# Kernel tuning notes

Hardware: AMD Instinct MI355X
Metric: run time of the kernel (lower is better)

## Reference

```python
import jax, jax.numpy as jnp
import numpy as np

N_ATOM = 30000
N_PAIR = 1_000_000
N_TRI = 4_000_000
N_SF = 16
RC = 6.0

LAMBD = jnp.array([-1.0, 1.0] * 8, dtype=jnp.float32)
ZETA = jnp.array([1.0, 1.0, 2.0, 2.0, 4.0, 4.0, 8.0, 8.0] * 2, dtype=jnp.float32)
ETA = jnp.array([0.01, 0.014, 0.02, 0.028, 0.04, 0.056, 0.08, 0.11,
                 0.16, 0.22, 0.32, 0.45, 0.63, 0.72, 0.9, 1.0], dtype=jnp.float32)


def cutoff_f1(r):
    # PiNN 'f1' cutoff: 0.5*(cos(pi*r/rc)+1)
    return 0.5 * (jnp.cos(jnp.float32(np.pi) * r / RC) + 1.0)


def gaussian_basis(r, fc):
    # GaussianBasis with center=0, gamma=eta: fc * exp(-eta * r^2), shape [n, n_sf]
    return fc[:, None] * jnp.exp(-ETA[None, :] * (r[:, None] ** 2))


def setup_inputs() -> dict:
    key = jax.random.key(0)
    k1, k2, k3, k4, k5 = jax.random.split(key, 5)
    ind_2 = jax.random.randint(k1, (N_PAIR, 2), 0, N_ATOM, dtype=jnp.int32)
    ind_3 = jax.random.randint(k2, (N_TRI, 2), 0, N_PAIR, dtype=jnp.int32)
    dist = jax.random.uniform(k3, (N_PAIR,), jnp.float32, 0.5, RC)
    dirs = jax.random.normal(k4, (N_PAIR, 3), jnp.float32)
    dirs = dirs / jnp.linalg.norm(dirs, axis=1, keepdims=True)
    diff = dirs * dist[:, None]  # bond vectors consistent with dist
    elems = jax.random.randint(k5, (N_ATOM,), 0, 4, dtype=jnp.int32)
    fc = cutoff_f1(dist)
    return {"ind_2": ind_2, "ind_3": ind_3, "dist": dist, "diff": diff,
            "elems": elems, "fc": fc}


def reference(ind_2, ind_3, dist, diff, elems, fc):
    # i=j=k='ALL': species filter is identity; a_rind = arange(n_atom)
    ind_ij = ind_3[:, 0]
    ind_ik = ind_3[:, 1]
    i_rind = ind_2[ind_ij, 0]  # central atom index per triplet

    diff_ij = diff[ind_ij]  # [T,3]
    diff_ik = diff[ind_ik]
    diff_jk = diff_ik - diff_ij
    dist_jk = jnp.linalg.norm(diff_jk, axis=1)
    mask = dist_jk < RC  # TF filters triplets; we mask (jit-friendly)

    fc_jk = cutoff_f1(dist_jk)
    dist_ij = dist[ind_ij]
    dist_ik = dist[ind_ik]
    fc_ij = fc[ind_ij]
    fc_ik = fc[ind_ik]

    cos_ijk = jnp.einsum('id,id->i', diff_ij, diff_ik) / dist_ij / dist_ik
    base = jnp.maximum(1.0 + LAMBD[None, :] * cos_ijk[:, None], 0.0)
    sf = (2.0 ** (1.0 - ZETA[None, :]) * base ** ZETA[None, :]
          * gaussian_basis(dist_ij, fc_ij)
          * gaussian_basis(dist_ik, fc_ik)
          * gaussian_basis(dist_jk, fc_jk))
    sf = jnp.where(mask[:, None], sf, 0.0)

    # scatter_nd add into per-atom fingerprints
    fp = jnp.zeros((N_ATOM, N_SF), dtype=sf.dtype).at[i_rind].add(sf)

    # jacobian indices: central-atom rel index per participating pair
    vals = jnp.where(mask, i_rind, -1)
    seg = jnp.concatenate([ind_ij, ind_ik])
    pair_i = jax.ops.segment_max(jnp.concatenate([vals, vals]), seg,
                                 num_segments=N_PAIR)
    pair_i = jnp.maximum(pair_i, -1)  # empty segments -> -1 sentinel
    jacob_ind = jnp.stack([jnp.arange(N_PAIR, dtype=jnp.int32), pair_i], axis=1)
    return fp, jacob_ind
```

## Files before the change

kernel.cpp:

```cpp
#include <hip/hip_runtime.h>

#define N_ATOM 30000
#define N_PAIR 1000000
#define N_TRI  4000000
#define N_SF   16
#define FP_ELEMS (N_ATOM * N_SF)

#define ASH  5
#define APB  32
#define NCB  938
#define NSUB 8
#define NSEG (NCB * NSUB)
#define OVF_CNT_IDX NSEG
#define OVF_CAP 131072
#define TILE 4096
#define PER_TH 16
#define NTILES ((N_TRI + TILE - 1) / TILE)
#define NWAVE 4

#define OFF_CCNT  0ULL
#define OFF_IKMAX 65536ULL
#define OFF_AOFP  4065536ULL
#define OFF_FLAG  6065536ULL
#define OFF_OVF   7065536ULL
#define OFF_PACK  8114112ULL
#define OFF_CB    24114112ULL

__device__ __forceinline__ bool tri_math_pack(
    float4 A, float4 B, float A8[8], float& R2)
{
    float ax = A.x, ay = A.y, az = A.z, fcij = A.w;
    float bx = B.x, by = B.y, bz = B.z, fcik = B.w;
    float d2ij = fmaf(ax, ax, fmaf(ay, ay, az * az));
    float d2ik = fmaf(bx, bx, fmaf(by, by, bz * bz));
    float jx = bx - ax, jy = by - ay, jz = bz - az;
    float d2jk = fmaf(jx, jx, fmaf(jy, jy, jz * jz));
    if (!(d2jk < 36.0f)) return false;
    float dij = sqrtf(d2ij);
    float dik = sqrtf(d2ik);
    float djk = sqrtf(d2jk);
    const float PI_OVER_RC = 0.5235987755982988f;
    float fcjk = 0.5f * (__cosf(PI_OVER_RC * djk) + 1.0f);
    float dot = fmaf(ax, bx, fmaf(ay, by, az * bz));
    float cosv = dot / (dij * dik);
    R2 = d2ij + d2ik + d2jk;
    float FCt = fcij * fcik * fcjk;
    float bm = fmaxf(1.0f - cosv, 0.0f);
    float bp = fmaxf(1.0f + cosv, 0.0f);
    float bm2 = bm * bm, bp2 = bp * bp;
    float bm4 = bm2 * bm2, bp4 = bp2 * bp2;
    float bm8 = bm4 * bm4, bp8 = bp4 * bp4;
    A8[0] = FCt * bm;              A8[1] = FCt * bp;
    A8[2] = 0.5f * FCt * bm2;      A8[3] = 0.5f * FCt * bp2;
    A8[4] = 0.125f * FCt * bm4;    A8[5] = 0.125f * FCt * bp4;
    A8[6] = 0.0078125f * FCt * bm8; A8[7] = 0.0078125f * FCt * bp8;
    return true;
}

#define SF_ACCUM(lrow, A8, R2, ATOMIC) do {                                   \
    float e0  = __expf(-0.01f  * (R2));                                       \
    float e1  = __expf(-0.014f * (R2));                                       \
    float e7  = __expf(-0.11f  * (R2));                                       \
    float e11 = __expf(-0.45f  * (R2));                                       \
    float e2 = e0*e0,  e3 = e1*e1;                                            \
    float e4 = e2*e2,  e5 = e3*e3;                                            \
    float e6 = e4*e4,  e9 = e7*e7;                                            \
    float e8 = e6*e6,  e14 = e11*e11;                                         \
    float e10 = e8*e8;                                                        \
    float e12 = e11*e8*e2;                                                    \
    float e13 = e10*e10*e6;                                                   \
    float e15 = e14*e6*e2;                                                    \
    ATOMIC(&(lrow)[0],  (A8)[0]*e0);  ATOMIC(&(lrow)[1],  (A8)[1]*e1);        \
    ATOMIC(&(lrow)[2],  (A8)[2]*e2);  ATOMIC(&(lrow)[3],  (A8)[3]*e3);        \
    ATOMIC(&(lrow)[4],  (A8)[4]*e4);  ATOMIC(&(lrow)[5],  (A8)[5]*e5);        \
    ATOMIC(&(lrow)[6],  (A8)[6]*e6);  ATOMIC(&(lrow)[7],  (A8)[7]*e7);        \
    ATOMIC(&(lrow)[8],  (A8)[0]*e8);  ATOMIC(&(lrow)[9],  (A8)[1]*e9);        \
    ATOMIC(&(lrow)[10], (A8)[2]*e10); ATOMIC(&(lrow)[11], (A8)[3]*e11);       \
    ATOMIC(&(lrow)[12], (A8)[4]*e12); ATOMIC(&(lrow)[13], (A8)[5]*e13);       \
    ATOMIC(&(lrow)[14], (A8)[6]*e14); ATOMIC(&(lrow)[15], (A8)[7]*e15);       \
} while (0)

#define ATOM_LDS(p, v)  atomicAdd((p), (v))
#define ATOM_GLB(p, v)  unsafeAtomicAdd((p), (v))


__global__ __launch_bounds__(256) void prep2(
    const int2* __restrict__ ind2, const float* __restrict__ diff,
    const float* __restrict__ fc,
    int* __restrict__ ccnt, int* __restrict__ ikmax,
    unsigned short* __restrict__ aofp, unsigned char* __restrict__ flag,
    float4* __restrict__ pack, float* __restrict__ out)
{
    int p = blockIdx.x * blockDim.x + threadIdx.x;
    if (p <= NSEG) ccnt[p] = 0;
    if (p < FP_ELEMS) out[p] = 0.0f;
    if (p >= N_PAIR) return;
    ikmax[p] = -1;
    flag[p] = 0;
    aofp[p] = (unsigned short)ind2[p].x;
    float4 r;
    r.x = diff[3 * p + 0];
    r.y = diff[3 * p + 1];
    r.z = diff[3 * p + 2];
    r.w = fc[p];
    pack[p] = r;
}

__global__ __launch_bounds__(256) void bin3(
    const int2* __restrict__ ind3, const unsigned short* __restrict__ aofp,
    int* __restrict__ ccnt, int2* __restrict__ cbucket,
    int2* __restrict__ ovf, int cap)
{
    __shared__ int lcnt[NCB];
    __shared__ int lbase[NCB];
    const int thr = threadIdx.x;
    const int sub = blockIdx.x & (NSUB - 1);
    const long long t0 = (long long)blockIdx.x * TILE;

    for (int i = thr; i < NCB; i += 256) lcnt[i] = 0;
    __syncthreads();

    int myatom[PER_TH];
    int myslot[PER_TH];
#pragma unroll
    for (int j = 0; j < PER_TH; ++j) {
        long long t = t0 + j * 256 + thr;
        int a = 0, s = -1;
        if (t < N_TRI) {
            int ij = ind3[t].x;
            a = aofp[ij];
            s = atomicAdd(&lcnt[a >> ASH], 1);
        }
        myatom[j] = a;
        myslot[j] = s;
    }
    __syncthreads();
    for (int c = thr; c < NCB; c += 256) {
        int n = lcnt[c];
        lbase[c] = n ? atomicAdd(&ccnt[c * NSUB + sub], n) : 0;
    }
    __syncthreads();
#pragma unroll
    for (int j = 0; j < PER_TH; ++j) {
        long long t = t0 + j * 256 + thr;
        if (t >= N_TRI) continue;
        int a = myatom[j];
        int c = a >> ASH;
        int slot = lbase[c] + myslot[j];
        int2 pr = ind3[t];
        if (slot < cap) {
            int2 e;
            e.x = pr.x | ((a & (APB - 1)) << 20);
            e.y = pr.y;
            cbucket[(size_t)(c * NSUB + sub) * cap + slot] = e;
        } else {
            int o = atomicAdd(&ccnt[OVF_CNT_IDX], 1);
            if (o < OVF_CAP) ovf[o] = pr;
        }
    }
}

__global__ __launch_bounds__(256) void reduce4(
    const int* __restrict__ ccnt, const int2* __restrict__ cbucket, int cap,
    const float4* __restrict__ pack,
    int* __restrict__ ikmax, unsigned char* __restrict__ flag,
    float* __restrict__ out)
{
    __shared__ float lacc[NWAVE][APB * 17];
    const int seg = blockIdx.x;
    const int b = seg >> 3;
    const int thr = threadIdx.x;
    const int wid = thr >> 6;
    for (int i = thr; i < NWAVE * APB * 17; i += 256)
        ((float*)lacc)[i] = 0.0f;
    __syncthreads();

    int n = ccnt[seg];
    n = min(n, cap);
    const int2* segp = cbucket + (size_t)seg * cap;
    for (int i = thr; i < n; i += 256) {
        int2 e = segp[i];
        int a5 = (e.x >> 20) & (APB - 1);
        int ij = e.x & 0xFFFFF;
        int ik = e.y;
        float4 A = pack[ij];
        float4 B = pack[ik];
        float A8[8], R2;
        if (!tri_math_pack(A, B, A8, R2)) continue;
        flag[ij] = 1;
        atomicMax(&ikmax[ik], (b << ASH) + a5);
        float* lrow = &lacc[wid][a5 * 17];
        SF_ACCUM(lrow, A8, R2, ATOM_LDS);
    }
    __syncthreads();
    for (int t = thr; t < APB * N_SF; t += 256) {
        int atom = (b << ASH) + (t >> 4);
        int idx = (t >> 4) * 17 + (t & 15);
        float v = lacc[0][idx] + lacc[1][idx] + lacc[2][idx] + lacc[3][idx];
        if (atom < N_ATOM && v != 0.0f)
            unsafeAtomicAdd(out + (size_t)atom * N_SF + (t & 15), v);
    }
}

__global__ __launch_bounds__(256) void ovf3(
    const int* __restrict__ ccnt, const int2* __restrict__ ovf,
    const float4* __restrict__ pack, const unsigned short* __restrict__ aofp,
    int* __restrict__ ikmax, unsigned char* __restrict__ flag,
    float* __restrict__ out)
{
    int i = blockIdx.x * blockDim.x + threadIdx.x;
    int n = ccnt[OVF_CNT_IDX];
    if (n > OVF_CAP) n = OVF_CAP;
    if (i >= n) return;
    int2 pr = ovf[i];
    int ij = pr.x, ik = pr.y;
    float A8[8], R2;
    if (!tri_math_pack(pack[ij], pack[ik], A8, R2)) return;
    int atom = aofp[ij];
    flag[ij] = 1;
    atomicMax(&ikmax[ik], atom);
    float* base = out + (size_t)atom * N_SF;
    SF_ACCUM(base, A8, R2, ATOM_GLB);
}

__global__ __launch_bounds__(256) void fin3(
    const int* __restrict__ ikmax, const unsigned char* __restrict__ flag,
    const unsigned short* __restrict__ aofp, float* __restrict__ out)
{
    int p = blockIdx.x * blockDim.x + threadIdx.x;
    if (p >= N_PAIR) return;
    int v = ikmax[p];
    if (flag[p]) { int a = aofp[p]; v = v > a ? v : a; }
    float* jf = out + FP_ELEMS;
    jf[2 * p + 0] = (float)p;
    jf[2 * p + 1] = (float)v;
}


__global__ __launch_bounds__(256) void init_legacy(float* __restrict__ out) {
    int i = blockIdx.x * blockDim.x + threadIdx.x;
    if (i < FP_ELEMS) out[i] = 0.0f;
    if (i < N_PAIR) ((int*)out + FP_ELEMS)[2 * i + 1] = -1;
}

__global__ __launch_bounds__(256) void tri_legacy(
    const int* __restrict__ ind2, const int2* __restrict__ ind3,
    const float* __restrict__ dist, const float* __restrict__ diff,
    const float* __restrict__ fc, float* __restrict__ out) {
    int t = blockIdx.x * blockDim.x + threadIdx.x;
    if (t >= N_TRI) return;
    int2 pr = ind3[t];
    int ij = pr.x, ik = pr.y;
    float4 A, B;
    A.x = diff[3 * ij + 0]; A.y = diff[3 * ij + 1]; A.z = diff[3 * ij + 2]; A.w = fc[ij];
    B.x = diff[3 * ik + 0]; B.y = diff[3 * ik + 1]; B.z = diff[3 * ik + 2]; B.w = fc[ik];
    float A8[8], R2;
    if (!tri_math_pack(A, B, A8, R2)) return;
    int atom = ind2[2 * ij];
    int* jac = (int*)out + FP_ELEMS;
    atomicMax(&jac[2 * ij + 1], atom);
    atomicMax(&jac[2 * ik + 1], atom);
    float* base = out + (size_t)atom * N_SF;
    SF_ACCUM(base, A8, R2, ATOM_GLB);
}

__global__ __launch_bounds__(256) void fin_legacy(float* __restrict__ out) {
    int p = blockIdx.x * blockDim.x + threadIdx.x;
    if (p >= N_PAIR) return;
    int* jac = (int*)out + FP_ELEMS;
    int v = jac[2 * p + 1];
    float* jf = (float*)jac;
    jf[2 * p + 0] = (float)p;
    jf[2 * p + 1] = (float)v;
}


extern "C" void kernel_launch(void* const* d_in, const int* in_sizes, int n_in,
                              void* d_out, int out_size, void* d_ws, size_t ws_size,
                              hipStream_t stream) {
    const int2*  ind2 = (const int2*)d_in[0];
    const int2*  ind3 = (const int2*)d_in[1];
    const float* dist = (const float*)d_in[2];
    const float* diff = (const float*)d_in[3];
    const float* fc   = (const float*)d_in[5];
    float* out = (float*)d_out;

    const size_t seg_stride = (size_t)NSEG * sizeof(int2);
    const size_t need_min = OFF_CB + seg_stride * 608;

    if (ws_size >= need_min) {
        char* ws = (char*)d_ws;
        int* ccnt            = (int*)(ws + OFF_CCNT);
        int* ikmax           = (int*)(ws + OFF_IKMAX);
        unsigned short* aofp = (unsigned short*)(ws + OFF_AOFP);
        unsigned char* flag  = (unsigned char*)(ws + OFF_FLAG);
        int2* ovf            = (int2*)(ws + OFF_OVF);
        float4* pack         = (float4*)(ws + OFF_PACK);
        int2* cbucket        = (int2*)(ws + OFF_CB);
        int cap = (int)((ws_size - OFF_CB) / seg_stride);
        if (cap > 1024) cap = 1024;

        int pb = (N_PAIR + 255) / 256;
        prep2<<<pb, 256, 0, stream>>>(ind2, diff, fc, ccnt, ikmax, aofp, flag, pack, out);
        bin3<<<NTILES, 256, 0, stream>>>(ind3, aofp, ccnt, cbucket, ovf, cap);
        reduce4<<<NSEG, 256, 0, stream>>>(ccnt, cbucket, cap, pack, ikmax, flag, out);
        ovf3<<<OVF_CAP / 256, 256, 0, stream>>>(ccnt, ovf, pack, aofp, ikmax, flag, out);
        fin3<<<pb, 256, 0, stream>>>(ikmax, flag, aofp, out);
    } else {
        init_legacy<<<(N_PAIR + 255) / 256, 256, 0, stream>>>(out);
        tri_legacy<<<(N_PAIR * 4 + 255) / 256, 256, 0, stream>>>((const int*)d_in[0], ind3, dist, diff, fc, out);
        fin_legacy<<<(N_PAIR + 255) / 256, 256, 0, stream>>>(out);
    }
    (void)dist; (void)in_sizes; (void)n_in; (void)out_size;
}
```

Baseline: 443.2 us.

## Quantize pair bond vectors to 20-bit packed coords, recompute cutoffs

Replaces the 16-byte float4 per-pair record (diff xyz plus fc) with an 8-byte record holding three 20-bit fixed-point coordinates, halving the bytes of each random gather in the triplet reduction. The cutoff factors fc_ij and fc_ik are recomputed from the decoded distances instead of being loaded. Triplets whose squared jk distance lies within a small epsilon of the cutoff are sent to the overflow path, which recomputes them exactly from the original float inputs, so the mask decision stays exact. In exchange it adds decode and cosine arithmetic, introduces quantization error in the fingerprints, and enlarges the bucket workspace, which may change cap.

```diff
diff --git a/kernel.cpp b/kernel.cpp
--- a/kernel.cpp
+++ b/kernel.cpp
@@ -24,9 +24,63 @@
 #define OFF_FLAG  6065536ULL
 #define OFF_OVF   7065536ULL
 #define OFF_PACK  8114112ULL
-#define OFF_CB    24114112ULL
-
-__device__ __forceinline__ bool tri_math_pack(
+#define OFF_CB    16114112ULL
+
+#define QSCALE 87381.333333f
+#define DQ     1.14440918e-5f
+#define EPS_D2 2.0e-3f
+
+__device__ __forceinline__ uint2 enc_pack(float x, float y, float z)
+{
+    unsigned qx = (unsigned)fminf(fmaxf(fmaf(x + 6.0f, QSCALE, 0.5f), 0.0f), 1048575.0f);
+    unsigned qy = (unsigned)fminf(fmaxf(fmaf(y + 6.0f, QSCALE, 0.5f), 0.0f), 1048575.0f);
+    unsigned qz = (unsigned)fminf(fmaxf(fmaf(z + 6.0f, QSCALE, 0.5f), 0.0f), 1048575.0f);
+    uint2 u;
+    u.x = qx | (qy << 20);
+    u.y = (qy >> 12) | (qz << 8);
+    return u;
+}
+
+__device__ __forceinline__ int tri_math_q(
+    uint2 U, uint2 V, float A8[8], float& R2)
+{
+    float ax = fmaf((float)(U.x & 0xFFFFF), DQ, -6.0f);
+    float ay = fmaf((float)(((U.x >> 20) | (U.y << 12)) & 0xFFFFF), DQ, -6.0f);
+    float az = fmaf((float)((U.y >> 8) & 0xFFFFF), DQ, -6.0f);
+    float bx = fmaf((float)(V.x & 0xFFFFF), DQ, -6.0f);
+    float by = fmaf((float)(((V.x >> 20) | (V.y << 12)) & 0xFFFFF), DQ, -6.0f);
+    float bz = fmaf((float)((V.y >> 8) & 0xFFFFF), DQ, -6.0f);
+    float d2ij = fmaf(ax, ax, fmaf(ay, ay, az * az));
+    float d2ik = fmaf(bx, bx, fmaf(by, by, bz * bz));
+    float jx = bx - ax, jy = by - ay, jz = bz - az;
+    float d2jk = fmaf(jx, jx, fmaf(jy, jy, jz * jz));
+    float dev = d2jk - 36.0f;
+    if (fabsf(dev) < EPS_D2) return 2;
+    if (dev > 0.0f) return 0;
+    float dij = sqrtf(d2ij);
+    float dik = sqrtf(d2ik);
+    float djk = sqrtf(d2jk);
+    const float PI_OVER_RC = 0.5235987755982988f;
+    float fcij = 0.5f * (__cosf(PI_OVER_RC * dij) + 1.0f);
+    float fcik = 0.5f * (__cosf(PI_OVER_RC * dik) + 1.0f);
+    float fcjk = 0.5f * (__cosf(PI_OVER_RC * djk) + 1.0f);
+    float dot = fmaf(ax, bx, fmaf(ay, by, az * bz));
+    float cosv = dot / (dij * dik);
+    R2 = d2ij + d2ik + d2jk;
+    float FCt = fcij * fcik * fcjk;
+    float bm = fmaxf(1.0f - cosv, 0.0f);
+    float bp = fmaxf(1.0f + cosv, 0.0f);
+    float bm2 = bm * bm, bp2 = bp * bp;
+    float bm4 = bm2 * bm2, bp4 = bp2 * bp2;
+    float bm8 = bm4 * bm4, bp8 = bp4 * bp4;
+    A8[0] = FCt * bm;              A8[1] = FCt * bp;
+    A8[2] = 0.5f * FCt * bm2;      A8[3] = 0.5f * FCt * bp2;
+    A8[4] = 0.125f * FCt * bm4;    A8[5] = 0.125f * FCt * bp4;
+    A8[6] = 0.0078125f * FCt * bm8; A8[7] = 0.0078125f * FCt * bp8;
+    return 1;
+}
+
+__device__ __forceinline__ bool tri_math_raw(
     float4 A, float4 B, float A8[8], float& R2)
 {
     float ax = A.x, ay = A.y, az = A.z, fcij = A.w;
@@ -86,10 +140,9 @@
 
 __global__ __launch_bounds__(256) void prep2(
     const int2* __restrict__ ind2, const float* __restrict__ diff,
-    const float* __restrict__ fc,
     int* __restrict__ ccnt, int* __restrict__ ikmax,
     unsigned short* __restrict__ aofp, unsigned char* __restrict__ flag,
-    float4* __restrict__ pack, float* __restrict__ out)
+    uint2* __restrict__ pack, float* __restrict__ out)
 {
     int p = blockIdx.x * blockDim.x + threadIdx.x;
     if (p <= NSEG) ccnt[p] = 0;
@@ -98,12 +151,7 @@
     ikmax[p] = -1;
     flag[p] = 0;
     aofp[p] = (unsigned short)ind2[p].x;
-    float4 r;
-    r.x = diff[3 * p + 0];
-    r.y = diff[3 * p + 1];
-    r.z = diff[3 * p + 2];
-    r.w = fc[p];
-    pack[p] = r;
+    pack[p] = enc_pack(diff[3 * p + 0], diff[3 * p + 1], diff[3 * p + 2]);
 }
 
 __global__ __launch_bounds__(256) void bin3(
@@ -162,8 +210,9 @@
 
 __global__ __launch_bounds__(256) void reduce4(
     const int* __restrict__ ccnt, const int2* __restrict__ cbucket, int cap,
-    const float4* __restrict__ pack,
+    const uint2* __restrict__ pack,
     int* __restrict__ ikmax, unsigned char* __restrict__ flag,
+    int* __restrict__ ovfcnt, int2* __restrict__ ovf,
     float* __restrict__ out)
 {
     __shared__ float lacc[NWAVE][APB * 17];
@@ -183,10 +232,16 @@
         int a5 = (e.x >> 20) & (APB - 1);
         int ij = e.x & 0xFFFFF;
         int ik = e.y;
-        float4 A = pack[ij];
-        float4 B = pack[ik];
+        uint2 U = pack[ij];
+        uint2 V = pack[ik];
         float A8[8], R2;
-        if (!tri_math_pack(A, B, A8, R2)) continue;
+        int code = tri_math_q(U, V, A8, R2);
+        if (code == 0) continue;
+        if (code == 2) {
+            int o = atomicAdd(ovfcnt, 1);
+            if (o < OVF_CAP) { int2 pr; pr.x = ij; pr.y = ik; ovf[o] = pr; }
+            continue;
+        }
         flag[ij] = 1;
         atomicMax(&ikmax[ik], (b << ASH) + a5);
         float* lrow = &lacc[wid][a5 * 17];
@@ -204,7 +259,8 @@
 
 __global__ __launch_bounds__(256) void ovf3(
     const int* __restrict__ ccnt, const int2* __restrict__ ovf,
-    const float4* __restrict__ pack, const unsigned short* __restrict__ aofp,
+    const float* __restrict__ diff, const float* __restrict__ fc,
+    const unsigned short* __restrict__ aofp,
     int* __restrict__ ikmax, unsigned char* __restrict__ flag,
     float* __restrict__ out)
 {
@@ -214,8 +270,11 @@
     if (i >= n) return;
     int2 pr = ovf[i];
     int ij = pr.x, ik = pr.y;
+    float4 A, B;
+    A.x = diff[3 * ij + 0]; A.y = diff[3 * ij + 1]; A.z = diff[3 * ij + 2]; A.w = fc[ij];
+    B.x = diff[3 * ik + 0]; B.y = diff[3 * ik + 1]; B.z = diff[3 * ik + 2]; B.w = fc[ik];
     float A8[8], R2;
-    if (!tri_math_pack(pack[ij], pack[ik], A8, R2)) return;
+    if (!tri_math_raw(A, B, A8, R2)) return;
     int atom = aofp[ij];
     flag[ij] = 1;
     atomicMax(&ikmax[ik], atom);
@@ -255,7 +314,7 @@
     A.x = diff[3 * ij + 0]; A.y = diff[3 * ij + 1]; A.z = diff[3 * ij + 2]; A.w = fc[ij];
     B.x = diff[3 * ik + 0]; B.y = diff[3 * ik + 1]; B.z = diff[3 * ik + 2]; B.w = fc[ik];
     float A8[8], R2;
-    if (!tri_math_pack(A, B, A8, R2)) return;
+    if (!tri_math_raw(A, B, A8, R2)) return;
     int atom = ind2[2 * ij];
     int* jac = (int*)out + FP_ELEMS;
     atomicMax(&jac[2 * ij + 1], atom);
@@ -295,20 +354,21 @@
         unsigned short* aofp = (unsigned short*)(ws + OFF_AOFP);
         unsigned char* flag  = (unsigned char*)(ws + OFF_FLAG);
         int2* ovf            = (int2*)(ws + OFF_OVF);
-        float4* pack         = (float4*)(ws + OFF_PACK);
+        uint2* pack          = (uint2*)(ws + OFF_PACK);
         int2* cbucket        = (int2*)(ws + OFF_CB);
         int cap = (int)((ws_size - OFF_CB) / seg_stride);
         if (cap > 1024) cap = 1024;
 
         int pb = (N_PAIR + 255) / 256;
-        prep2<<<pb, 256, 0, stream>>>(ind2, diff, fc, ccnt, ikmax, aofp, flag, pack, out);
+        prep2<<<pb, 256, 0, stream>>>(ind2, diff, ccnt, ikmax, aofp, flag, pack, out);
         bin3<<<NTILES, 256, 0, stream>>>(ind3, aofp, ccnt, cbucket, ovf, cap);
-        reduce4<<<NSEG, 256, 0, stream>>>(ccnt, cbucket, cap, pack, ikmax, flag, out);
-        ovf3<<<OVF_CAP / 256, 256, 0, stream>>>(ccnt, ovf, pack, aofp, ikmax, flag, out);
+        reduce4<<<NSEG, 256, 0, stream>>>(ccnt, cbucket, cap, pack, ikmax, flag,
+                                          &ccnt[OVF_CNT_IDX], ovf, out);
+        ovf3<<<OVF_CAP / 256, 256, 0, stream>>>(ccnt, ovf, diff, fc, aofp, ikmax, flag, out);
         fin3<<<pb, 256, 0, stream>>>(ikmax, flag, aofp, out);
     } else {
         init_legacy<<<(N_PAIR + 255) / 256, 256, 0, stream>>>(out);
-        tri_legacy<<<(N_PAIR * 4 + 255) / 256, 256, 0, stream>>>((const int*)d_in[0], ind3, dist, diff, fc, out);
+        tri_legacy<<<(N_TRI + 255) / 256, 256, 0, stream>>>((const int*)d_in[0], ind3, dist, diff, fc, out);
         fin_legacy<<<(N_PAIR + 255) / 256, 256, 0, stream>>>(out);
     }
     (void)dist; (void)in_sizes; (void)n_in; (void)out_size;
```

Result: no change. 443.9 us (+0.2%).
